# Kernel optimization log

Hardware: AMD Instinct MI355X
Metric: run time of the kernel (lower is better)

Reference implementation:

```python
import jax, jax.numpy as jnp
import numpy as np

EPS = 0.05
THRESH = 1e-6
MAX_ITER = 100


def _l2norm(x):
    # matches torch F.normalize(dim=-1): x / max(||x||, 1e-12)
    n = jnp.sqrt(jnp.sum(x * x, axis=-1, keepdims=True))
    return x / jnp.maximum(n, 1e-12)


def setup_inputs() -> dict:
    key = jax.random.key(0)
    kq, kk, kv = jax.random.split(key, 3)
    B, N, D = 8, 1024, 64
    return {
        "q": jax.random.normal(kq, (B, N, D), dtype=jnp.float32),
        "k": jax.random.normal(kk, (B, N, D), dtype=jnp.float32),
        "V": jax.random.normal(kv, (B, N, D), dtype=jnp.float32),
    }


def reference(q, k, V):
    B, N, D = q.shape
    Q = _l2norm(q)
    Kn = _l2norm(k)
    # cost matrix: 1 - cosine similarity, shape (B, N, N)
    C = 1.0 - jnp.einsum("bnd,bmd->bnm", Q, Kn)

    log_mu = jnp.full((B, N), jnp.log(1.0 / N + 1e-8), dtype=C.dtype)
    log_nu = log_mu

    def kernel(u, v):
        # (-C + u_i + v_j) / eps, shape (B, N, N)
        return (-C + u[:, :, None] + v[:, None, :]) / EPS

    def step(carry, _):
        u, v, done = carry
        u0 = u
        u_new = EPS * (log_mu - jax.scipy.special.logsumexp(kernel(u, v), axis=2)) + u
        v_new = EPS * (log_nu - jax.scipy.special.logsumexp(kernel(u_new, v), axis=1)) + v
        err = jnp.mean(jnp.abs(u_new - u0))
        # replicate torch early-break: once converged, freeze u, v
        u = jnp.where(done, u, u_new)
        v = jnp.where(done, v, v_new)
        done = jnp.logical_or(done, err < THRESH)
        return (u, v, done), None

    u0 = jnp.zeros((B, N), dtype=C.dtype)
    v0 = jnp.zeros((B, N), dtype=C.dtype)
    (u, v, _), _ = jax.lax.scan(
        jax.checkpoint(step), (u0, v0, jnp.array(False)), None, length=MAX_ITER
    )

    T = jnp.exp(kernel(u, v))  # transport plan (B, N, N)
    out = jnp.einsum("bnm,bmd->bnd", T, V) + V
    return out
```

## Files before the change

### kernel.cpp

```cpp
#include <hip/hip_runtime.h>
#include <math.h>

#define BB 8
#define NN 1024
#define DD 64
#define EPSF 0.05f
#define MAX_ITER 100
#define ERR_FX_THRESH 8590u
#define SCALE_ 28.853900817779268f
#define EPSLN2_ 0.034657359027997264f
#define NBLK 256
#define NPER 32

typedef __attribute__((ext_vector_type(8))) short short8;
typedef __attribute__((ext_vector_type(4))) float f32x4;

static __device__ __forceinline__ float fexp2(float x) { return __builtin_amdgcn_exp2f(x); }
static __device__ __forceinline__ float flog2(float x) { return __builtin_amdgcn_logf(x); }
static __device__ __forceinline__ float bflo(unsigned u) { return __uint_as_float(u << 16); }
static __device__ __forceinline__ unsigned short bf16rne(float x) {
    unsigned u = __float_as_uint(x);
    u += 0x7fffu + ((u >> 16) & 1u);
    return (unsigned short)(u >> 16);
}
__device__ __forceinline__ float wave_sum64(float x) {
#pragma unroll
    for (int off = 1; off < 64; off <<= 1) x += __shfl_xor(x, off);
    return x;
}

#define CNT64IDX(p, b) ((b) * 200 + (p))

__global__ __launch_bounds__(256) void cost_kernel(const float* __restrict__ q,
                                                   const float* __restrict__ k,
                                                   unsigned short* __restrict__ M,
                                                   unsigned short* __restrict__ MT) {
    __shared__ __align__(16) float Qs[64][65];
    __shared__ __align__(16) float Ks[64][65];
    __shared__ float qin[64];
    __shared__ float kin[64];
    __shared__ __align__(16) unsigned short Qb[64][72];
    __shared__ __align__(16) unsigned short Kb[64][72];
    int b = blockIdx.z;
    int i0 = blockIdx.y * 64, j0 = blockIdx.x * 64;
    const float* Qp = q + ((size_t)b * NN + i0) * DD;
    const float* Kp = k + ((size_t)b * NN + j0) * DD;
    int tid = threadIdx.x;
#pragma unroll
    for (int kk = 0; kk < 4; ++kk) {
        int c = tid + 256 * kk;
        int row = c >> 4;
        int c4 = c & 15;
        float4 qv = ((const float4*)(Qp + row * DD))[c4];
        Qs[row][c4 * 4 + 0] = qv.x; Qs[row][c4 * 4 + 1] = qv.y;
        Qs[row][c4 * 4 + 2] = qv.z; Qs[row][c4 * 4 + 3] = qv.w;
        float4 kv = ((const float4*)(Kp + row * DD))[c4];
        Ks[row][c4 * 4 + 0] = kv.x; Ks[row][c4 * 4 + 1] = kv.y;
        Ks[row][c4 * 4 + 2] = kv.z; Ks[row][c4 * 4 + 3] = kv.w;
    }
    __syncthreads();
    if (tid < 64) {
        float ss = 0.f;
#pragma unroll 16
        for (int d = 0; d < 64; ++d) ss += Qs[tid][d] * Qs[tid][d];
        qin[tid] = 1.0f / fmaxf(sqrtf(ss), 1e-12f);
    } else if (tid < 128) {
        int r = tid - 64;
        float ss = 0.f;
#pragma unroll 16
        for (int d = 0; d < 64; ++d) ss += Ks[r][d] * Ks[r][d];
        kin[r] = 1.0f / fmaxf(sqrtf(ss), 1e-12f);
    }
    __syncthreads();
    {
        int row = tid >> 2, d0 = (tid & 3) * 16;
        float qs = qin[row], ks = kin[row];
#pragma unroll
        for (int p = 0; p < 4; ++p) {
            int d = d0 + p * 4;
            uint2 t;
            t.x = (unsigned)bf16rne(Qs[row][d + 0] * qs) | ((unsigned)bf16rne(Qs[row][d + 1] * qs) << 16);
            t.y = (unsigned)bf16rne(Qs[row][d + 2] * qs) | ((unsigned)bf16rne(Qs[row][d + 3] * qs) << 16);
            *(uint2*)&Qb[row][d] = t;
            t.x = (unsigned)bf16rne(Ks[row][d + 0] * ks) | ((unsigned)bf16rne(Ks[row][d + 1] * ks) << 16);
            t.y = (unsigned)bf16rne(Ks[row][d + 2] * ks) | ((unsigned)bf16rne(Ks[row][d + 3] * ks) << 16);
            *(uint2*)&Kb[row][d] = t;
        }
    }
    __syncthreads();
    unsigned short* Ms  = (unsigned short*)&Qs[0][0];
    unsigned short* MsT = (unsigned short*)&Ks[0][0];
    int w = tid >> 6, lane = tid & 63;
    int m = lane & 15, qq = lane >> 4;
    int rloc = w * 16;
    short8 a0 = *(const short8*)&Qb[rloc + m][qq * 8];
    short8 a1 = *(const short8*)&Qb[rloc + m][qq * 8 + 32];
    f32x4 acc[4];
#pragma unroll
    for (int nt = 0; nt < 4; ++nt) {
        short8 b0 = *(const short8*)&Kb[nt * 16 + m][qq * 8];
        short8 b1 = *(const short8*)&Kb[nt * 16 + m][qq * 8 + 32];
        f32x4 z = {0.f, 0.f, 0.f, 0.f};
        z = __builtin_amdgcn_mfma_f32_16x16x32_bf16(a0, b0, z, 0, 0, 0);
        acc[nt] = __builtin_amdgcn_mfma_f32_16x16x32_bf16(a1, b1, z, 0, 0, 0);
    }
#pragma unroll
    for (int nt = 0; nt < 4; ++nt) {
        unsigned short us[4];
#pragma unroll
        for (int r = 0; r < 4; ++r)
            us[r] = bf16rne(fexp2((acc[nt][r] - 1.0f) * SCALE_));
#pragma unroll
        for (int r = 0; r < 4; ++r)
            Ms[(rloc + qq * 4 + r) * 72 + nt * 16 + m] = us[r];
        uint2 t;
        t.x = (unsigned)us[0] | ((unsigned)us[1] << 16);
        t.y = (unsigned)us[2] | ((unsigned)us[3] << 16);
        *(uint2*)&MsT[(nt * 16 + m) * 72 + rloc + qq * 4] = t;
    }
    __syncthreads();
#pragma unroll
    for (int s = 0; s < 2; ++s) {
        int idx = tid + 256 * s;
        int row = idx >> 3, seg = idx & 7;
        *(uint4*)(M + ((size_t)b << 20) + ((size_t)(i0 + row) << 10) + j0 + seg * 8) =
            *(const uint4*)&Ms[row * 72 + seg * 8];
        *(uint4*)(MT + ((size_t)b << 20) + ((size_t)(j0 + row) << 10) + i0 + seg * 8) =
            *(const uint4*)&MsT[row * 72 + seg * 8];
    }
}

#define ACC8(U4, base)                                              \
    s0 = fmaf(bflo(U4.x), wrg[base + 0], s0);                       \
    s1 = fmaf(__uint_as_float(U4.x), wrg[base + 1], s1);            \
    s0 = fmaf(bflo(U4.y), wrg[base + 2], s0);                       \
    s1 = fmaf(__uint_as_float(U4.y), wrg[base + 3], s1);            \
    s0 = fmaf(bflo(U4.z), wrg[base + 4], s0);                       \
    s1 = fmaf(__uint_as_float(U4.z), wrg[base + 5], s1);            \
    s0 = fmaf(bflo(U4.w), wrg[base + 6], s0);                       \
    s1 = fmaf(__uint_as_float(U4.w), wrg[base + 7], s1);

__global__ __launch_bounds__(256, 1) void sink_coop(const unsigned short* __restrict__ M,
                                                    const unsigned short* __restrict__ MT,
                                                    float* __restrict__ u,
                                                    float* __restrict__ v,
                                                    unsigned long long* __restrict__ cnt64,
                                                    float eln) {
    __shared__ __align__(16) float sw[1280];
    __shared__ float sdel[4];
    __shared__ int sflag;
    int tid = threadIdx.x;
    int w = tid >> 6, lane = tid & 63;
    int b = blockIdx.x & 7;
    int slice = blockIdx.x >> 3;
    int rbase = slice * 32 + w * 8;
    const unsigned short* Mb  = M  + ((size_t)b << 20);
    const unsigned short* MTb = MT + ((size_t)b << 20);
    float* ub = u + (b << 10);
    float* vb = v + (b << 10);

    uint4 mA[8], mB[8], nA[8], nB[8];
#pragma unroll
    for (int r = 0; r < 8; ++r) {
        const uint4* rp = (const uint4*)(Mb + ((size_t)(rbase + r) << 10));
        mA[r] = rp[lane * 2];
        mB[r] = rp[lane * 2 + 1];
        const uint4* tp = (const uint4*)(MTb + ((size_t)(rbase + r) << 10));
        nA[r] = tp[lane * 2];
        nB[r] = tp[lane * 2 + 1];
    }

    float uprev[8];
#pragma unroll
    for (int r = 0; r < 8; ++r) uprev[r] = 0.f;

    unsigned myerr = 0xffffffffu;

    for (int t = 0; t < MAX_ITER; ++t) {
        {
            float4 ex;
            ex.x = fexp2(__hip_atomic_load(vb + tid * 4 + 0, __ATOMIC_RELAXED, __HIP_MEMORY_SCOPE_AGENT) * SCALE_);
            ex.y = fexp2(__hip_atomic_load(vb + tid * 4 + 1, __ATOMIC_RELAXED, __HIP_MEMORY_SCOPE_AGENT) * SCALE_);
            ex.z = fexp2(__hip_atomic_load(vb + tid * 4 + 2, __ATOMIC_RELAXED, __HIP_MEMORY_SCOPE_AGENT) * SCALE_);
            ex.w = fexp2(__hip_atomic_load(vb + tid * 4 + 3, __ATOMIC_RELAXED, __HIP_MEMORY_SCOPE_AGENT) * SCALE_);
            *(float4*)&sw[tid * 4 + 4 * (tid >> 2)] = ex;
            __syncthreads();
            float wrg[16];
            *(float4*)&wrg[0]  = *(const float4*)&sw[lane * 20 + 0];
            *(float4*)&wrg[4]  = *(const float4*)&sw[lane * 20 + 4];
            *(float4*)&wrg[8]  = *(const float4*)&sw[lane * 20 + 8];
            *(float4*)&wrg[12] = *(const float4*)&sw[lane * 20 + 12];
            float del = 0.f;
#pragma unroll
            for (int rr = 0; rr < 8; ++rr) {
                float s0 = 0.f, s1 = 0.f;
                ACC8(mA[rr], 0)
                ACC8(mB[rr], 8)
                float s = wave_sum64(s0 + s1);
                float un = eln - EPSLN2_ * flog2(s);
                del += fabsf(un - uprev[rr]);
                uprev[rr] = un;
                if (lane == 0)
                    __hip_atomic_store(ub + rbase + rr, un, __ATOMIC_RELAXED, __HIP_MEMORY_SCOPE_AGENT);
            }
            if (lane == 0) sdel[w] = del;
            asm volatile("s_waitcnt vmcnt(0)" ::: "memory");
            __syncthreads();
            if (tid == 0) {
                float dsum = sdel[0] + sdel[1] + sdel[2] + sdel[3];
                unsigned dfx = (unsigned)fminf(dsum * 1048576.0f, 6.0e7f) + 1u;
                unsigned long long* c = cnt64 + CNT64IDX(2 * t, b);
                unsigned long long tot =
                    __hip_atomic_fetch_add(c, (1ULL << 32) | (unsigned long long)dfx,
                                           __ATOMIC_RELAXED, __HIP_MEMORY_SCOPE_AGENT) +
                    ((1ULL << 32) | (unsigned long long)dfx);
                while ((unsigned)(tot >> 32) < NPER) {
                    __builtin_amdgcn_s_sleep(1);
                    tot = __hip_atomic_load(c, __ATOMIC_RELAXED, __HIP_MEMORY_SCOPE_AGENT);
                }
                myerr = (unsigned)tot;
            }
            __syncthreads();
        }
        {
            float4 ex;
            ex.x = fexp2(__hip_atomic_load(ub + tid * 4 + 0, __ATOMIC_RELAXED, __HIP_MEMORY_SCOPE_AGENT) * SCALE_);
            ex.y = fexp2(__hip_atomic_load(ub + tid * 4 + 1, __ATOMIC_RELAXED, __HIP_MEMORY_SCOPE_AGENT) * SCALE_);
            ex.z = fexp2(__hip_atomic_load(ub + tid * 4 + 2, __ATOMIC_RELAXED, __HIP_MEMORY_SCOPE_AGENT) * SCALE_);
            ex.w = fexp2(__hip_atomic_load(ub + tid * 4 + 3, __ATOMIC_RELAXED, __HIP_MEMORY_SCOPE_AGENT) * SCALE_);
            *(float4*)&sw[tid * 4 + 4 * (tid >> 2)] = ex;
            __syncthreads();
            float wrg[16];
            *(float4*)&wrg[0]  = *(const float4*)&sw[lane * 20 + 0];
            *(float4*)&wrg[4]  = *(const float4*)&sw[lane * 20 + 4];
            *(float4*)&wrg[8]  = *(const float4*)&sw[lane * 20 + 8];
            *(float4*)&wrg[12] = *(const float4*)&sw[lane * 20 + 12];
#pragma unroll
            for (int rr = 0; rr < 8; ++rr) {
                float s0 = 0.f, s1 = 0.f;
                ACC8(nA[rr], 0)
                ACC8(nB[rr], 8)
                float s = wave_sum64(s0 + s1);
                float vn = eln - EPSLN2_ * flog2(s);
                if (lane == 0)
                    __hip_atomic_store(vb + rbase + rr, vn, __ATOMIC_RELAXED, __HIP_MEMORY_SCOPE_AGENT);
            }
            asm volatile("s_waitcnt vmcnt(0)" ::: "memory");
            __syncthreads();
            if (tid == 0) {
                unsigned long long* c = cnt64 + CNT64IDX(2 * t + 1, b);
                unsigned long long tot =
                    __hip_atomic_fetch_add(c, 1ULL << 32, __ATOMIC_RELAXED, __HIP_MEMORY_SCOPE_AGENT) +
                    (1ULL << 32);
                while ((unsigned)(tot >> 32) < NPER) {
                    __builtin_amdgcn_s_sleep(1);
                    tot = __hip_atomic_load(c, __ATOMIC_RELAXED, __HIP_MEMORY_SCOPE_AGENT);
                }
                int brk = 0;
                if (myerr < ERR_FX_THRESH) {
                    unsigned long long s = 0;
                    for (int bb = 0; bb < 8; ++bb) {
                        unsigned long long tv = __hip_atomic_load(cnt64 + CNT64IDX(2 * t, bb),
                                                                  __ATOMIC_RELAXED, __HIP_MEMORY_SCOPE_AGENT);
                        while ((unsigned)(tv >> 32) < NPER) {
                            __builtin_amdgcn_s_sleep(1);
                            tv = __hip_atomic_load(cnt64 + CNT64IDX(2 * t, bb),
                                                   __ATOMIC_RELAXED, __HIP_MEMORY_SCOPE_AGENT);
                        }
                        s += (unsigned long long)(unsigned)tv;
                    }
                    brk = (s < (unsigned long long)ERR_FX_THRESH);
                }
                sflag = brk;
            }
            __syncthreads();
            if (sflag) break;
        }
    }
}

__global__ __launch_bounds__(256) void wt_kernel(const float* __restrict__ V,
                                                 const float* __restrict__ v,
                                                 unsigned short* __restrict__ WT) {
    __shared__ __align__(16) float Vs[64][65];
    __shared__ float wj[64];
    int b = blockIdx.x & 7, jt = blockIdx.x >> 3;
    int j0 = jt * 64;
    int tid = threadIdx.x;
    const float* Vb = V + ((size_t)b << 16) + ((size_t)j0 << 6);
#pragma unroll
    for (int c = 0; c < 4; ++c) {
        int idx = tid + 256 * c;
        int row = idx >> 4, c4 = idx & 15;
        float4 x = ((const float4*)(Vb + row * 64))[c4];
        Vs[row][c4 * 4 + 0] = x.x; Vs[row][c4 * 4 + 1] = x.y;
        Vs[row][c4 * 4 + 2] = x.z; Vs[row][c4 * 4 + 3] = x.w;
    }
    if (tid < 64) wj[tid] = fexp2(v[(b << 10) + j0 + tid] * SCALE_);
    __syncthreads();
    int d = tid >> 2, qd = tid & 3;
    unsigned pk[8];
#pragma unroll
    for (int p = 0; p < 8; ++p) {
        int j = qd * 16 + p * 2;
        unsigned lo = bf16rne(Vs[j][d] * wj[j]);
        unsigned hi = bf16rne(Vs[j + 1][d] * wj[j + 1]);
        pk[p] = lo | (hi << 16);
    }
    unsigned short* dst = WT + ((size_t)b << 16) + ((size_t)d << 10) + j0 + qd * 16;
    ((uint4*)dst)[0] = make_uint4(pk[0], pk[1], pk[2], pk[3]);
    ((uint4*)dst)[1] = make_uint4(pk[4], pk[5], pk[6], pk[7]);
}

__global__ __launch_bounds__(256) void gemm_final(const unsigned short* __restrict__ M,
                                                  const unsigned short* __restrict__ WT,
                                                  const float* __restrict__ u,
                                                  const float* __restrict__ V,
                                                  float* __restrict__ out) {
    __shared__ float sa[32];
    int tid = threadIdx.x;
    int w = tid >> 6, lane = tid & 63;
    int b = blockIdx.x & 7, mt = blockIdx.x >> 3;
    if (tid < 32) sa[tid] = fexp2(u[(b << 10) + mt * 32 + tid] * SCALE_);
    __syncthreads();
    int m = lane & 15, q = lane >> 4;
    int rloc = (w & 1) * 16;
    int nbase = (w >> 1) * 32;
    const unsigned short* Ma = M + ((size_t)b << 20) + ((size_t)(mt * 32 + rloc + m) << 10) + q * 8;
    const unsigned short* W0 = WT + ((size_t)b << 16) + ((size_t)(nbase + m) << 10) + q * 8;
    const unsigned short* W1 = W0 + (16 << 10);
    f32x4 acc0 = {0.f, 0.f, 0.f, 0.f}, acc1 = {0.f, 0.f, 0.f, 0.f};
#pragma unroll 4
    for (int k0 = 0; k0 < NN; k0 += 32) {
        short8 af = *(const short8*)(Ma + k0);
        short8 b0 = *(const short8*)(W0 + k0);
        short8 b1 = *(const short8*)(W1 + k0);
        acc0 = __builtin_amdgcn_mfma_f32_16x16x32_bf16(af, b0, acc0, 0, 0, 0);
        acc1 = __builtin_amdgcn_mfma_f32_16x16x32_bf16(af, b1, acc1, 0, 0, 0);
    }
#pragma unroll
    for (int r = 0; r < 4; ++r) {
        int lrow = rloc + q * 4 + r;
        int gm = mt * 32 + lrow;
        float a = sa[lrow];
        size_t base = (((size_t)b << 10) + gm) * DD;
        int n0 = nbase + m;
        out[base + n0]      = fmaf(a, acc0[r], V[base + n0]);
        out[base + n0 + 16] = fmaf(a, acc1[r], V[base + n0 + 16]);
    }
}

extern "C" void kernel_launch(void* const* d_in, const int* in_sizes, int n_in,
                              void* d_out, int out_size, void* d_ws, size_t ws_size,
                              hipStream_t stream) {
    const float* q = (const float*)d_in[0];
    const float* k = (const float*)d_in[1];
    const float* V = (const float*)d_in[2];
    float* out = (float*)d_out;

    char* ws = (char*)d_ws;
    const size_t MB16 = (size_t)BB * NN * NN * sizeof(unsigned short);
    unsigned short* M  = (unsigned short*)ws;
    unsigned short* MT = (unsigned short*)(ws + MB16);
    unsigned short* WT = MT;
    float* u   = (float*)(ws + 2 * MB16);
    float* v   = u + BB * NN;
    unsigned long long* cnt64 = (unsigned long long*)(v + BB * NN);

    size_t zbytes = (size_t)(2 * BB * NN) * 4 + 1600 * 8;
    hipMemsetAsync(u, 0, zbytes, stream);

    cost_kernel<<<dim3(16, 16, 8), 256, 0, stream>>>(q, k, M, MT);

    float eln = EPSF * logf(1.0f / NN + 1e-8f);
    sink_coop<<<dim3(NBLK), dim3(256), 0, stream>>>(M, MT, u, v, cnt64, eln);

    wt_kernel<<<128, 256, 0, stream>>>(V, v, WT);
    gemm_final<<<256, 256, 0, stream>>>(M, WT, u, V, out);
}
```

Before: 185.9 us.

## Replace atomic-counter grid barrier with per-wave epoch-tagged slot flags

The per-batch barrier based on a 64-bit atomic fetch_add counter is replaced by per-wave slot words tagged with the iteration number. Wave 0 of each block polls all 128 slots in parallel with a wave-wide __all. Error partials are packed into the slot words, and a per-iteration errlog carries the per-batch error for the global convergence check. This removes the atomic RMW contention, and two of the block-level __syncthreads plus the single-thread spin. In exchange it adds polling traffic, and the packed fixed-point fields are narrower.

```diff
diff --git a/kernel.cpp b/kernel.cpp
--- a/kernel.cpp
+++ b/kernel.cpp
@@ -6,11 +6,10 @@
 #define DD 64
 #define EPSF 0.05f
 #define MAX_ITER 100
-#define ERR_FX_THRESH 8590u
+#define ERRF_THRESH 8590.0f
 #define SCALE_ 28.853900817779268f
 #define EPSLN2_ 0.034657359027997264f
 #define NBLK 256
-#define NPER 32
 
 typedef __attribute__((ext_vector_type(8))) short short8;
 typedef __attribute__((ext_vector_type(4))) float f32x4;
@@ -29,7 +28,6 @@
     return x;
 }
 
-#define CNT64IDX(p, b) ((b) * 200 + (p))
 
 __global__ __launch_bounds__(256) void cost_kernel(const float* __restrict__ q,
                                                    const float* __restrict__ k,
@@ -144,10 +142,10 @@
                                                     const unsigned short* __restrict__ MT,
                                                     float* __restrict__ u,
                                                     float* __restrict__ v,
-                                                    unsigned long long* __restrict__ cnt64,
+                                                    unsigned* __restrict__ slots,
+                                                    unsigned* __restrict__ errlog,
                                                     float eln) {
     __shared__ __align__(16) float sw[1280];
-    __shared__ float sdel[4];
     __shared__ int sflag;
     int tid = threadIdx.x;
     int w = tid >> 6, lane = tid & 63;
@@ -158,6 +156,9 @@
     const unsigned short* MTb = MT + ((size_t)b << 20);
     float* ub = u + (b << 10);
     float* vb = v + (b << 10);
+    unsigned* slu = slots + b * 256;
+    unsigned* slv = slu + 128;
+    int myslot = slice * 4 + w;
 
     uint4 mA[8], mB[8], nA[8], nB[8];
 #pragma unroll
@@ -174,9 +175,10 @@
 #pragma unroll
     for (int r = 0; r < 8; ++r) uprev[r] = 0.f;
 
-    unsigned myerr = 0xffffffffu;
+    float myerr = 1e30f;
 
     for (int t = 0; t < MAX_ITER; ++t) {
+        unsigned tg = (unsigned)(t + 1);
         {
             float4 ex;
             ex.x = fexp2(__hip_atomic_load(vb + tid * 4 + 0, __ATOMIC_RELAXED, __HIP_MEMORY_SCOPE_AGENT) * SCALE_);
@@ -203,22 +205,29 @@
                 if (lane == 0)
                     __hip_atomic_store(ub + rbase + rr, un, __ATOMIC_RELAXED, __HIP_MEMORY_SCOPE_AGENT);
             }
-            if (lane == 0) sdel[w] = del;
             asm volatile("s_waitcnt vmcnt(0)" ::: "memory");
-            __syncthreads();
-            if (tid == 0) {
-                float dsum = sdel[0] + sdel[1] + sdel[2] + sdel[3];
-                unsigned dfx = (unsigned)fminf(dsum * 1048576.0f, 6.0e7f) + 1u;
-                unsigned long long* c = cnt64 + CNT64IDX(2 * t, b);
-                unsigned long long tot =
-                    __hip_atomic_fetch_add(c, (1ULL << 32) | (unsigned long long)dfx,
-                                           __ATOMIC_RELAXED, __HIP_MEMORY_SCOPE_AGENT) +
-                    ((1ULL << 32) | (unsigned long long)dfx);
-                while ((unsigned)(tot >> 32) < NPER) {
+            if (lane == 0) {
+                unsigned dfx = (unsigned)fminf(del * 1048576.0f, 3.0e7f) + 1u;
+                __hip_atomic_store(slu + myslot, (tg << 25) | dfx,
+                                   __ATOMIC_RELAXED, __HIP_MEMORY_SCOPE_AGENT);
+            }
+            if (w == 0) {
+                const unsigned* p0 = slu + lane * 2;
+                float es;
+                for (;;) {
+                    unsigned s0 = __hip_atomic_load(p0, __ATOMIC_RELAXED, __HIP_MEMORY_SCOPE_AGENT);
+                    unsigned s1 = __hip_atomic_load(p0 + 1, __ATOMIC_RELAXED, __HIP_MEMORY_SCOPE_AGENT);
+                    if (__all(((s0 >> 25) == tg) && ((s1 >> 25) == tg))) {
+                        es = (float)(s0 & 0x1FFFFFFu) + (float)(s1 & 0x1FFFFFFu);
+                        break;
+                    }
                     __builtin_amdgcn_s_sleep(1);
-                    tot = __hip_atomic_load(c, __ATOMIC_RELAXED, __HIP_MEMORY_SCOPE_AGENT);
                 }
-                myerr = (unsigned)tot;
+                myerr = wave_sum64(es);
+                if (slice == 0 && lane == 0)
+                    __hip_atomic_store(errlog + t * 8 + b,
+                                       (tg << 25) | (unsigned)fminf(myerr, 3.3e7f),
+                                       __ATOMIC_RELAXED, __HIP_MEMORY_SCOPE_AGENT);
             }
             __syncthreads();
         }
@@ -246,32 +255,33 @@
                     __hip_atomic_store(vb + rbase + rr, vn, __ATOMIC_RELAXED, __HIP_MEMORY_SCOPE_AGENT);
             }
             asm volatile("s_waitcnt vmcnt(0)" ::: "memory");
-            __syncthreads();
-            if (tid == 0) {
-                unsigned long long* c = cnt64 + CNT64IDX(2 * t + 1, b);
-                unsigned long long tot =
-                    __hip_atomic_fetch_add(c, 1ULL << 32, __ATOMIC_RELAXED, __HIP_MEMORY_SCOPE_AGENT) +
-                    (1ULL << 32);
-                while ((unsigned)(tot >> 32) < NPER) {
+            if (lane == 0)
+                __hip_atomic_store(slv + myslot, tg << 25,
+                                   __ATOMIC_RELAXED, __HIP_MEMORY_SCOPE_AGENT);
+            if (w == 0) {
+                const unsigned* p0 = slv + lane * 2;
+                for (;;) {
+                    unsigned s0 = __hip_atomic_load(p0, __ATOMIC_RELAXED, __HIP_MEMORY_SCOPE_AGENT);
+                    unsigned s1 = __hip_atomic_load(p0 + 1, __ATOMIC_RELAXED, __HIP_MEMORY_SCOPE_AGENT);
+                    if (__all(((s0 >> 25) == tg) && ((s1 >> 25) == tg))) break;
                     __builtin_amdgcn_s_sleep(1);
-                    tot = __hip_atomic_load(c, __ATOMIC_RELAXED, __HIP_MEMORY_SCOPE_AGENT);
                 }
                 int brk = 0;
-                if (myerr < ERR_FX_THRESH) {
-                    unsigned long long s = 0;
+                if (myerr < ERRF_THRESH) {
+                    float gs = 0.f;
                     for (int bb = 0; bb < 8; ++bb) {
-                        unsigned long long tv = __hip_atomic_load(cnt64 + CNT64IDX(2 * t, bb),
-                                                                  __ATOMIC_RELAXED, __HIP_MEMORY_SCOPE_AGENT);
-                        while ((unsigned)(tv >> 32) < NPER) {
+                        unsigned wv;
+                        for (;;) {
+                            wv = __hip_atomic_load(errlog + t * 8 + bb,
+                                                   __ATOMIC_RELAXED, __HIP_MEMORY_SCOPE_AGENT);
+                            if ((wv >> 25) == tg) break;
                             __builtin_amdgcn_s_sleep(1);
-                            tv = __hip_atomic_load(cnt64 + CNT64IDX(2 * t, bb),
-                                                   __ATOMIC_RELAXED, __HIP_MEMORY_SCOPE_AGENT);
                         }
-                        s += (unsigned long long)(unsigned)tv;
+                        gs += (float)(wv & 0x1FFFFFFu);
                     }
-                    brk = (s < (unsigned long long)ERR_FX_THRESH);
+                    brk = (gs < ERRF_THRESH);
                 }
-                sflag = brk;
+                if (lane == 0) sflag = brk;
             }
             __syncthreads();
             if (sflag) break;
@@ -365,15 +375,16 @@
     unsigned short* WT = MT;
     float* u   = (float*)(ws + 2 * MB16);
     float* v   = u + BB * NN;
-    unsigned long long* cnt64 = (unsigned long long*)(v + BB * NN);
-
-    size_t zbytes = (size_t)(2 * BB * NN) * 4 + 1600 * 8;
+    unsigned* slots  = (unsigned*)(v + BB * NN);
+    unsigned* errlog = slots + 2048;
+
+    size_t zbytes = (size_t)(2 * BB * NN + 2048 + 800) * 4;
     hipMemsetAsync(u, 0, zbytes, stream);
 
     cost_kernel<<<dim3(16, 16, 8), 256, 0, stream>>>(q, k, M, MT);
 
     float eln = EPSF * logf(1.0f / NN + 1e-8f);
-    sink_coop<<<dim3(NBLK), dim3(256), 0, stream>>>(M, MT, u, v, cnt64, eln);
+    sink_coop<<<dim3(NBLK), dim3(256), 0, stream>>>(M, MT, u, v, slots, errlog, eln);
 
     wt_kernel<<<128, 256, 0, stream>>>(V, v, WT);
     gemm_final<<<256, 256, 0, stream>>>(M, WT, u, V, out);
```

After: 266.8 us. 1.44x slower.

## Fuse weight prep and final GEMM into persistent Sinkhorn kernel

Applied to the files above, without the earlier changes.

Removes the separate wt_kernel and gemm_final launches. After convergence, each sink_coop block rebuilds the scaled, transposed bf16 V weights for its batch in LDS (about 132KB) and runs the MFMA GEMM for its 32-row slice, writing the output directly. The host memset of v and the counters is replaced by zeroing done in one block of cost_kernel. This saves launch gaps and the global WT round trip. In exchange, every block redundantly recomputes the per-batch weight matrix, LDS use becomes large, and correctness relies on v being globally visible after the final sync.

```diff
diff --git a/kernel.cpp b/kernel.cpp
--- a/kernel.cpp
+++ b/kernel.cpp
@@ -11,6 +11,7 @@
 #define EPSLN2_ 0.034657359027997264f
 #define NBLK 256
 #define NPER 32
+#define WPITCH 1032
 
 typedef __attribute__((ext_vector_type(8))) short short8;
 typedef __attribute__((ext_vector_type(4))) float f32x4;
@@ -34,7 +35,8 @@
 __global__ __launch_bounds__(256) void cost_kernel(const float* __restrict__ q,
                                                    const float* __restrict__ k,
                                                    unsigned short* __restrict__ M,
-                                                   unsigned short* __restrict__ MT) {
+                                                   unsigned short* __restrict__ MT,
+                                                   float* __restrict__ vz) {
     __shared__ __align__(16) float Qs[64][65];
     __shared__ __align__(16) float Ks[64][65];
     __shared__ float qin[64];
@@ -46,6 +48,10 @@
     const float* Qp = q + ((size_t)b * NN + i0) * DD;
     const float* Kp = k + ((size_t)b * NN + j0) * DD;
     int tid = threadIdx.x;
+    if (blockIdx.x == 0 && blockIdx.y == 0 && blockIdx.z == 0) {
+        float4 z4 = {0.f, 0.f, 0.f, 0.f};
+        for (int i = tid; i < 2848; i += 256) ((float4*)vz)[i] = z4;
+    }
 #pragma unroll
     for (int kk = 0; kk < 4; ++kk) {
         int c = tid + 256 * kk;
@@ -145,10 +151,16 @@
                                                     float* __restrict__ u,
                                                     float* __restrict__ v,
                                                     unsigned long long* __restrict__ cnt64,
+                                                    const float* __restrict__ V,
+                                                    float* __restrict__ out,
                                                     float eln) {
     __shared__ __align__(16) float sw[1280];
     __shared__ float sdel[4];
     __shared__ int sflag;
+    __shared__ __align__(16) float Vs[64][65];
+    __shared__ float wj[64];
+    __shared__ float sa[32];
+    __shared__ __align__(16) unsigned short Wl[64 * WPITCH];
     int tid = threadIdx.x;
     int w = tid >> 6, lane = tid & 63;
     int b = blockIdx.x & 7;
@@ -277,76 +289,75 @@
             if (sflag) break;
         }
     }
-}
-
-__global__ __launch_bounds__(256) void wt_kernel(const float* __restrict__ V,
-                                                 const float* __restrict__ v,
-                                                 unsigned short* __restrict__ WT) {
-    __shared__ __align__(16) float Vs[64][65];
-    __shared__ float wj[64];
-    int b = blockIdx.x & 7, jt = blockIdx.x >> 3;
-    int j0 = jt * 64;
-    int tid = threadIdx.x;
-    const float* Vb = V + ((size_t)b << 16) + ((size_t)j0 << 6);
-#pragma unroll
-    for (int c = 0; c < 4; ++c) {
-        int idx = tid + 256 * c;
-        int row = idx >> 4, c4 = idx & 15;
-        float4 x = ((const float4*)(Vb + row * 64))[c4];
-        Vs[row][c4 * 4 + 0] = x.x; Vs[row][c4 * 4 + 1] = x.y;
-        Vs[row][c4 * 4 + 2] = x.z; Vs[row][c4 * 4 + 3] = x.w;
-    }
-    if (tid < 64) wj[tid] = fexp2(v[(b << 10) + j0 + tid] * SCALE_);
-    __syncthreads();
-    int d = tid >> 2, qd = tid & 3;
-    unsigned pk[8];
-#pragma unroll
-    for (int p = 0; p < 8; ++p) {
-        int j = qd * 16 + p * 2;
-        unsigned lo = bf16rne(Vs[j][d] * wj[j]);
-        unsigned hi = bf16rne(Vs[j + 1][d] * wj[j + 1]);
-        pk[p] = lo | (hi << 16);
-    }
-    unsigned short* dst = WT + ((size_t)b << 16) + ((size_t)d << 10) + j0 + qd * 16;
-    ((uint4*)dst)[0] = make_uint4(pk[0], pk[1], pk[2], pk[3]);
-    ((uint4*)dst)[1] = make_uint4(pk[4], pk[5], pk[6], pk[7]);
-}
-
-__global__ __launch_bounds__(256) void gemm_final(const unsigned short* __restrict__ M,
-                                                  const unsigned short* __restrict__ WT,
-                                                  const float* __restrict__ u,
-                                                  const float* __restrict__ V,
-                                                  float* __restrict__ out) {
-    __shared__ float sa[32];
-    int tid = threadIdx.x;
-    int w = tid >> 6, lane = tid & 63;
-    int b = blockIdx.x & 7, mt = blockIdx.x >> 3;
-    if (tid < 32) sa[tid] = fexp2(u[(b << 10) + mt * 32 + tid] * SCALE_);
-    __syncthreads();
-    int m = lane & 15, q = lane >> 4;
-    int rloc = (w & 1) * 16;
-    int nbase = (w >> 1) * 32;
-    const unsigned short* Ma = M + ((size_t)b << 20) + ((size_t)(mt * 32 + rloc + m) << 10) + q * 8;
-    const unsigned short* W0 = WT + ((size_t)b << 16) + ((size_t)(nbase + m) << 10) + q * 8;
-    const unsigned short* W1 = W0 + (16 << 10);
-    f32x4 acc0 = {0.f, 0.f, 0.f, 0.f}, acc1 = {0.f, 0.f, 0.f, 0.f};
+
+    {
+#pragma unroll
+        for (int r = 0; r < 8; ++r)
+            if (lane == r) sa[w * 8 + r] = fexp2(uprev[r] * SCALE_);
+
+        const float* Vbase = V + ((size_t)b << 16);
+        float4 pv[4];
+#pragma unroll
+        for (int c = 0; c < 4; ++c) pv[c] = ((const float4*)Vbase)[tid + 256 * c];
+
+        for (int jp = 0; jp < 16; ++jp) {
+            __syncthreads();
+#pragma unroll
+            for (int c = 0; c < 4; ++c) {
+                int idx = tid + 256 * c;
+                int row = idx >> 4, c4 = idx & 15;
+                Vs[row][c4 * 4 + 0] = pv[c].x; Vs[row][c4 * 4 + 1] = pv[c].y;
+                Vs[row][c4 * 4 + 2] = pv[c].z; Vs[row][c4 * 4 + 3] = pv[c].w;
+            }
+            if (tid < 64)
+                wj[tid] = fexp2(__hip_atomic_load(vb + jp * 64 + tid,
+                                                  __ATOMIC_RELAXED, __HIP_MEMORY_SCOPE_AGENT) * SCALE_);
+            __syncthreads();
+            if (jp < 15) {
+                const float* Vnp = Vbase + (size_t)(jp + 1) * 4096;
+#pragma unroll
+                for (int c = 0; c < 4; ++c) pv[c] = ((const float4*)Vnp)[tid + 256 * c];
+            }
+            int d = tid >> 2, qd = tid & 3;
+            unsigned pk[8];
+#pragma unroll
+            for (int p = 0; p < 8; ++p) {
+                int j = qd * 16 + p * 2;
+                unsigned lo = bf16rne(Vs[j][d] * wj[j]);
+                unsigned hi = bf16rne(Vs[j + 1][d] * wj[j + 1]);
+                pk[p] = lo | (hi << 16);
+            }
+            unsigned short* dst = &Wl[(size_t)d * WPITCH + jp * 64 + qd * 16];
+            ((uint4*)dst)[0] = make_uint4(pk[0], pk[1], pk[2], pk[3]);
+            ((uint4*)dst)[1] = make_uint4(pk[4], pk[5], pk[6], pk[7]);
+        }
+        __syncthreads();
+
+        int m = lane & 15, q = lane >> 4;
+        int rloc = (w & 1) * 16;
+        int nbase = (w >> 1) * 32;
+        const unsigned short* Ma = M + ((size_t)b << 20) + ((size_t)(slice * 32 + rloc + m) << 10) + q * 8;
+        const unsigned short* W0 = &Wl[(size_t)(nbase + m) * WPITCH + q * 8];
+        const unsigned short* W1 = W0 + 16 * WPITCH;
+        f32x4 acc0 = {0.f, 0.f, 0.f, 0.f}, acc1 = {0.f, 0.f, 0.f, 0.f};
 #pragma unroll 4
-    for (int k0 = 0; k0 < NN; k0 += 32) {
-        short8 af = *(const short8*)(Ma + k0);
-        short8 b0 = *(const short8*)(W0 + k0);
-        short8 b1 = *(const short8*)(W1 + k0);
-        acc0 = __builtin_amdgcn_mfma_f32_16x16x32_bf16(af, b0, acc0, 0, 0, 0);
-        acc1 = __builtin_amdgcn_mfma_f32_16x16x32_bf16(af, b1, acc1, 0, 0, 0);
-    }
-#pragma unroll
-    for (int r = 0; r < 4; ++r) {
-        int lrow = rloc + q * 4 + r;
-        int gm = mt * 32 + lrow;
-        float a = sa[lrow];
-        size_t base = (((size_t)b << 10) + gm) * DD;
-        int n0 = nbase + m;
-        out[base + n0]      = fmaf(a, acc0[r], V[base + n0]);
-        out[base + n0 + 16] = fmaf(a, acc1[r], V[base + n0 + 16]);
+        for (int k0 = 0; k0 < NN; k0 += 32) {
+            short8 af = *(const short8*)(Ma + k0);
+            short8 b0 = *(const short8*)(W0 + k0);
+            short8 b1 = *(const short8*)(W1 + k0);
+            acc0 = __builtin_amdgcn_mfma_f32_16x16x32_bf16(af, b0, acc0, 0, 0, 0);
+            acc1 = __builtin_amdgcn_mfma_f32_16x16x32_bf16(af, b1, acc1, 0, 0, 0);
+        }
+#pragma unroll
+        for (int r = 0; r < 4; ++r) {
+            int lrow = rloc + q * 4 + r;
+            int gm = slice * 32 + lrow;
+            float a = sa[lrow];
+            size_t base = (((size_t)b << 10) + gm) * DD;
+            int n0 = nbase + m;
+            out[base + n0]      = fmaf(a, acc0[r], V[base + n0]);
+            out[base + n0 + 16] = fmaf(a, acc1[r], V[base + n0 + 16]);
+        }
     }
 }
 
@@ -362,19 +373,12 @@
     const size_t MB16 = (size_t)BB * NN * NN * sizeof(unsigned short);
     unsigned short* M  = (unsigned short*)ws;
     unsigned short* MT = (unsigned short*)(ws + MB16);
-    unsigned short* WT = MT;
     float* u   = (float*)(ws + 2 * MB16);
     float* v   = u + BB * NN;
     unsigned long long* cnt64 = (unsigned long long*)(v + BB * NN);
 
-    size_t zbytes = (size_t)(2 * BB * NN) * 4 + 1600 * 8;
-    hipMemsetAsync(u, 0, zbytes, stream);
-
-    cost_kernel<<<dim3(16, 16, 8), 256, 0, stream>>>(q, k, M, MT);
+    cost_kernel<<<dim3(16, 16, 8), 256, 0, stream>>>(q, k, M, MT, v);
 
     float eln = EPSF * logf(1.0f / NN + 1e-8f);
-    sink_coop<<<dim3(NBLK), dim3(256), 0, stream>>>(M, MT, u, v, cnt64, eln);
-
-    wt_kernel<<<128, 256, 0, stream>>>(V, v, WT);
-    gemm_final<<<256, 256, 0, stream>>>(M, WT, u, V, out);
-}
+    sink_coop<<<dim3(NBLK), dim3(256), 0, stream>>>(M, MT, u, v, cnt64, V, out, eln);
+}
```

Measured after the change: 186.6 us. No clear change (+0.4%).
